# Kernel optimization log

Hardware: AMD Instinct MI355X
Metric: run time of the kernel (lower is better)

Reference implementation:

```python
import jax, jax.numpy as jnp
import numpy as np

N = 100000
E = 3200000
IN_DIM = 3
HID = 256
OUT_DIM = 3


def setup_inputs() -> dict:
    key = jax.random.key(0)
    ks = jax.random.split(key, 12)
    x = jax.random.normal(ks[0], (N, IN_DIM), dtype=jnp.float32)
    edge_index = jax.random.randint(ks[1], (2, E), 0, N, dtype=jnp.int64)
    def lin(k, fi, fo):
        k1, k2 = jax.random.split(k)
        bound = 1.0 / np.sqrt(fi)
        W = jax.random.uniform(k1, (fi, fo), jnp.float32, -bound, bound)
        b = jax.random.uniform(k2, (fo,), jnp.float32, -bound, bound)
        return W, b
    W0, b0 = lin(ks[2], IN_DIM, HID)
    W1, b1 = lin(ks[3], HID, HID)
    W2, b2 = lin(ks[4], HID, HID)
    W3, b3 = lin(ks[5], HID, OUT_DIM)
    Wr, br = lin(ks[6], IN_DIM, OUT_DIM)
    return {"x": x, "edge_index": edge_index,
            "W0": W0, "b0": b0, "W1": W1, "b1": b1,
            "W2": W2, "b2": b2, "W3": W3, "b3": b3,
            "Wr": Wr, "br": br}


def reference(x, edge_index, W0, b0, W1, b1, W2, b2, W3, b3, Wr, br):
    n = x.shape[0]
    # add self loops, mirroring build_adjacency_matrix
    loops = jnp.arange(n, dtype=edge_index.dtype)
    row = jnp.concatenate([edge_index[0], loops])
    col = jnp.concatenate([edge_index[1], loops])
    # degree of row endpoints, D^{-1/2}[row] * D^{-1/2}[col] edge weights
    deg = jax.ops.segment_sum(jnp.ones_like(row, dtype=x.dtype), row, num_segments=n)
    dinv = jnp.where(deg > 0, jax.lax.rsqrt(deg), 0.0)
    norm = dinv[row] * dinv[col]  # [E+N]

    def propagate(h):
        # A_hat @ h : gather source features, scale, scatter-add to rows
        return jax.ops.segment_sum(norm[:, None] * h[col], row, num_segments=n)

    h = jax.nn.relu(propagate(x) @ W0 + b0)
    h = jax.nn.relu(propagate(h) @ W1 + b1)
    h = jax.nn.relu(propagate(h) @ W2 + b2)
    h = propagate(h) @ W3 + b3  # last layer: no relu
    return h + (x @ Wr + br)
```

## Files before the change

### kernel.cpp

```cpp
#include <hip/hip_runtime.h>
#include <stdint.h>

typedef unsigned short u16;
typedef unsigned int u32;
typedef __attribute__((ext_vector_type(8))) short short8;
typedef __attribute__((ext_vector_type(4))) float f32x4;
typedef __attribute__((ext_vector_type(2))) unsigned int u32x2;

#define CAP 6144
#define TILE 4096

__device__ __forceinline__ float b2f_bits(u32 bits){ union{u32 u; float f;} v; v.u=bits; return v.f; }
__device__ __forceinline__ float bf_lo(u32 w){ return b2f_bits(w<<16); }
__device__ __forceinline__ float bf_hi(u32 w){ return b2f_bits(w & 0xffff0000u); }
__device__ __forceinline__ u16 f2bf(float f){
  union{float f; u32 u;} v; v.f=f;
  return (u16)((v.u + 0x7fffu + ((v.u>>16)&1u))>>16);
}


__global__ void detect_k(const long long* __restrict__ ei, int* __restrict__ flag,
                         int* __restrict__ gcur, int n, int E, int nbuck){
  __shared__ int sh[256];
  int t = threadIdx.x;
  for(int i=t; i<nbuck; i+=256) gcur[i]=0;
  int lim = E/2 < 2048 ? E/2 : 2048;
  int bad = 0;
  for(int e=t; e<lim; e+=256){
    unsigned long long v = (unsigned long long)ei[e];
    if(v >= (unsigned long long)n) bad = 1;
  }
  sh[t]=bad; __syncthreads();
  for(int off=128; off>0; off>>=1){ if(t<off) sh[t] |= sh[t+off]; __syncthreads(); }
  if(t==0) *flag = sh[0];
}

__device__ __forceinline__ int edge_at(const void* eiv, int is32, long long idx){
  return is32 ? ((const int*)eiv)[idx] : (int)((const long long*)eiv)[idx];
}
__device__ __forceinline__ int clampi(int v, int lo, int hi){
  return v < lo ? lo : (v > hi ? hi : v);
}

__global__ __launch_bounds__(256) void binA_k(const void* __restrict__ eiv, const int* __restrict__ flag,
                        int* __restrict__ gcur, u32* __restrict__ gbuf, int E, int n, int nbuck){
  __shared__ int hist[1024];
  __shared__ int base[1024];
  __shared__ int cur[1024];
  __shared__ int wsum[256];
  __shared__ u32 stage[TILE];
  int t = threadIdx.x;
  long long e0 = (long long)blockIdx.x * TILE;
  int cnt = (int)((long long)E - e0 < TILE ? (long long)E - e0 : TILE);
  int is32 = *flag;
  for(int i=t; i<nbuck; i+=256){ hist[i]=0; cur[i]=0; }
  __syncthreads();
  int eb[16]; u32 ep[16]; int ec=0;
  #pragma unroll
  for(int k=0;k<16;k++){
    int i = t + k*256;
    if(i<cnt){
      long long e = e0 + i;
      int r = clampi(edge_at(eiv,is32,e),0,n-1);
      int c = clampi(edge_at(eiv,is32,(long long)E+e),0,n-1);
      eb[ec] = r>>7;
      ep[ec] = ((u32)(r&127)<<17) | (u32)c;
      atomicAdd(&hist[eb[ec]],1);
      ec++;
    }
  }
  __syncthreads();
  int l[4]; int tot=0;
  #pragma unroll
  for(int j=0;j<4;j++){ int idx=t*4+j; l[j]=(idx<nbuck)?hist[idx]:0; tot+=l[j]; }
  wsum[t]=tot; __syncthreads();
  for(int off=1;off<256;off<<=1){
    int x = (t>=off)?wsum[t-off]:0;
    __syncthreads();
    wsum[t]+=x;
    __syncthreads();
  }
  int excl = wsum[t]-tot;
  #pragma unroll
  for(int j=0;j<4;j++){ int idx=t*4+j; if(idx<nbuck) base[idx]=excl; excl+=l[j]; }
  __syncthreads();
  for(int k=0;k<ec;k++){
    int b = eb[k];
    int slot = base[b] + atomicAdd(&cur[b],1);
    stage[slot] = ep[k];
  }
  __syncthreads();
  for(int b=t; b<nbuck; b+=256){
    int c = hist[b];
    if(c>0){
      int g = atomicAdd(&gcur[b], c);
      if(g > CAP) g = CAP;
      if(g + c > CAP) c = CAP - g;
      int src = base[b];
      u32* dst = gbuf + (size_t)b*CAP + g;
      for(int k=0;k<c;k++) dst[k] = stage[src+k];
    }
  }
}

__global__ __launch_bounds__(256) void scanG_k(const int* __restrict__ gcnt, int* __restrict__ gstart, int nbuck){
  __shared__ int sh[256];
  int t = threadIdx.x;
  int v[4]; int s=0;
  #pragma unroll
  for(int j=0;j<4;j++){
    int idx=t*4+j;
    int c = (idx<nbuck)?gcnt[idx]:0;
    if(c>CAP) c=CAP;
    v[j]=c; s+=c;
  }
  sh[t]=s; __syncthreads();
  for(int off=1;off<256;off<<=1){
    int x=(t>=off)?sh[t-off]:0;
    __syncthreads();
    sh[t]+=x;
    __syncthreads();
  }
  int excl = sh[t]-s;
  #pragma unroll
  for(int j=0;j<4;j++){ int idx=t*4+j; if(idx<nbuck) gstart[idx]=excl; excl+=v[j]; }
}

__global__ __launch_bounds__(256) void csrB_k(const int* __restrict__ gcnt, const int* __restrict__ gstart,
                        const u32* __restrict__ gbuf, int* __restrict__ deg, float* __restrict__ dinv,
                        int* __restrict__ rs, int* __restrict__ csr, int n, int nbuck){
  __shared__ int h[128], lst[128], lcur[128], sc[128];
  __shared__ int colstage[CAP];
  int b = blockIdx.x, t = threadIdx.x;
  if(t<128){ h[t]=0; lcur[t]=0; }
  __syncthreads();
  int c = gcnt[b]; if(c>CAP) c=CAP;
  const u32* p = gbuf + (size_t)b*CAP;
  for(int i=t;i<c;i+=256) atomicAdd(&h[p[i]>>17],1);
  __syncthreads();
  int dv=0;
  if(t<128){ dv=h[t]; sc[t]=dv; }
  __syncthreads();
  for(int off=1;off<128;off<<=1){
    int x=(t>=off&&t<128)?sc[t-off]:0;
    __syncthreads();
    if(t<128) sc[t]+=x;
    __syncthreads();
  }
  int g0 = gstart[b];
  if(t<128){
    lst[t]=sc[t]-dv;
    int row=b*128+t;
    if(row<n){
      deg[row]=dv;
      dinv[row]=rsqrtf((float)(dv+1));
      rs[row]=g0+lst[t];
    }
  }
  __syncthreads();
  for(int i=t;i<c;i+=256){
    u32 pr=p[i];
    int rl=pr>>17;
    int slot=lst[rl]+atomicAdd(&lcur[rl],1);
    if(slot<CAP) colstage[slot]=(int)(pr&0x1FFFFu);
  }
  __syncthreads();
  for(int i=t;i<c;i+=256) csr[g0+i]=colstage[i];
}

__global__ void pack2_k(const float* __restrict__ W1, const float* __restrict__ W2,
                        u16* __restrict__ o1, u16* __restrict__ o2){
  int bid = blockIdx.x;
  const float* W = (bid<256)? W1 : W2;
  u16* out = (bid<256)? o1 : o2;
  int idx = (bid&255)*256 + threadIdx.x;
  int j  = idx & 7;
  int l  = (idx>>3) & 63;
  int ct = (idx>>9) & 15;
  int kk = idx>>13;
  int k  = kk*32 + (l>>4)*8 + j;
  int nn = ct*16 + (l&15);
  out[idx] = f2bf(W[k*256 + nn]);
}

__global__ void prop3_k(const float* __restrict__ x, const int* __restrict__ csr,
                        const int* __restrict__ rs, const int* __restrict__ deg,
                        const float* __restrict__ dinv, float* __restrict__ p0, int n){
  int i = blockIdx.x*256 + threadIdx.x;
  if(i>=n) return;
  float a0=0.f, a1=0.f, a2=0.f;
  int s = rs[i], e = s + deg[i];
  for(int t=s; t<e; t++){
    int c = csr[t];
    float w = dinv[c];
    a0 += w*x[c*3+0]; a1 += w*x[c*3+1]; a2 += w*x[c*3+2];
  }
  float di = dinv[i];
  a0 += di*x[i*3+0]; a1 += di*x[i*3+1]; a2 += di*x[i*3+2];
  p0[i*3+0]=di*a0; p0[i*3+1]=di*a1; p0[i*3+2]=di*a2;
}

__global__ __launch_bounds__(256) void prop256_k(const u16* __restrict__ hin, u16* __restrict__ pout,
                          const int* __restrict__ csr, const int* __restrict__ rs,
                          const int* __restrict__ deg, const float* __restrict__ dinv, int n){
  int row = (blockIdx.x*256 + threadIdx.x) >> 6;
  if(row>=n) return;
  row = __builtin_amdgcn_readfirstlane(row);
  int lane = threadIdx.x & 63;
  int co = lane*4;
  const u16* hb = hin + co;
  uint2 sv = *(const uint2*)(hb + (size_t)row*256);
  float a0=bf_lo(sv.x), a1=bf_hi(sv.x), a2=bf_lo(sv.y), a3=bf_hi(sv.y);
  int s = __builtin_amdgcn_readfirstlane(rs[row]);
  int d = __builtin_amdgcn_readfirstlane(deg[row]);
  for(int base=0; base<d; base+=16){
    int cc[16]; u32 mk[16];
    #pragma unroll
    for(int j=0;j<16;j++){
      int ok = (base+j) < d;
      cc[j] = csr[ok ? (s+base+j) : s];
      mk[j] = ok ? 0xffffffffu : 0u;
    }
    uint2 v[16];
    #pragma unroll
    for(int j=0;j<16;j++) v[j] = *(const uint2*)(hb + (size_t)cc[j]*256);
    #pragma unroll
    for(int j=0;j<16;j++){
      u32 xw = v[j].x & mk[j], yw = v[j].y & mk[j];
      a0 += bf_lo(xw); a1 += bf_hi(xw); a2 += bf_lo(yw); a3 += bf_hi(yw);
    }
  }
  float sc = dinv[row];
  u32x2 o;
  o.x = (u32)f2bf(a0*sc) | ((u32)f2bf(a1*sc)<<16);
  o.y = (u32)f2bf(a2*sc) | ((u32)f2bf(a3*sc)<<16);
  __builtin_nontemporal_store(o, (u32x2*)(pout + (size_t)row*256 + co));
}

__global__ __launch_bounds__(256) void gemm0_k(const float* __restrict__ p0, const float* __restrict__ W0,
                        const float* __restrict__ b0, const float* __restrict__ dinv,
                        u16* __restrict__ h1, int n){
  int i = blockIdx.x;
  int j = threadIdx.x;
  float v = p0[i*3+0]*W0[j] + p0[i*3+1]*W0[256+j] + p0[i*3+2]*W0[512+j] + b0[j];
  v = fmaxf(v, 0.f) * dinv[i];
  h1[(size_t)i*256 + j] = f2bf(v);
}

__global__ __launch_bounds__(256) void gemm256_k(const u16* __restrict__ A, const u16* __restrict__ Bp,
                          const float* __restrict__ bias, const float* __restrict__ dinv,
                          u16* __restrict__ Out, int M){
  int wave = threadIdx.x>>6, lane = threadIdx.x&63;
  int rowbase = blockIdx.x*64 + wave*16;
  f32x4 acc[16];
  #pragma unroll
  for(int t=0;t<16;t++){ acc[t][0]=0.f; acc[t][1]=0.f; acc[t][2]=0.f; acc[t][3]=0.f; }
  const u16* Ap = A + (size_t)(rowbase + (lane&15))*256 + ((lane>>4)*8);
  const u16* Bl = Bp + (size_t)lane*8;
  #pragma unroll
  for(int kk=0; kk<8; kk++){
    short8 af = __builtin_nontemporal_load((const short8*)(Ap + kk*32));
    const u16* bb = Bl + (size_t)kk*8192;
    #pragma unroll
    for(int t=0;t<16;t++){
      short8 bf = *(const short8*)(bb + t*512);
      acc[t] = __builtin_amdgcn_mfma_f32_16x16x32_bf16(af, bf, acc[t], 0, 0, 0);
    }
  }
  int r0 = rowbase + (lane>>4)*4;
  float dv[4]; bool ok[4];
  #pragma unroll
  for(int r=0;r<4;r++){ ok[r] = (r0+r) < M; dv[r] = ok[r] ? dinv[r0+r] : 0.f; }
  #pragma unroll
  for(int t=0;t<16;t++){
    int col = t*16 + (lane&15);
    float bc = bias[col];
    #pragma unroll
    for(int r=0;r<4;r++){
      if(ok[r]){
        float v = fmaxf(acc[t][r] + bc, 0.f) * dv[r];
        Out[(size_t)(r0+r)*256 + col] = f2bf(v);
      }
    }
  }
}

__global__ __launch_bounds__(256) void gemm3_k(const u16* __restrict__ h3, const float* __restrict__ W3,
                        float* __restrict__ qh, int n){
  __shared__ float w3s[768];
  for(int i=threadIdx.x; i<768; i+=256) w3s[i] = W3[i];
  __syncthreads();
  int i = blockIdx.x*256 + threadIdx.x;
  if(i>=n) return;
  float a0=0.f, a1=0.f, a2=0.f;
  const uint4* hp = (const uint4*)(h3 + (size_t)i*256);
  for(int kk=0; kk<32; kk++){
    uint4 v = hp[kk];
    float f[8] = {bf_lo(v.x),bf_hi(v.x),bf_lo(v.y),bf_hi(v.y),
                  bf_lo(v.z),bf_hi(v.z),bf_lo(v.w),bf_hi(v.w)};
    int k0 = kk*8;
    #pragma unroll
    for(int j=0;j<8;j++){
      a0 += f[j]*w3s[(k0+j)*3+0];
      a1 += f[j]*w3s[(k0+j)*3+1];
      a2 += f[j]*w3s[(k0+j)*3+2];
    }
  }
  qh[i*3+0]=a0; qh[i*3+1]=a1; qh[i*3+2]=a2;
}

__global__ void final_k(const float* __restrict__ qh, const float* __restrict__ x,
                        const int* __restrict__ csr, const int* __restrict__ rs,
                        const int* __restrict__ deg, const float* __restrict__ dinv,
                        const float* __restrict__ b3, const float* __restrict__ Wr,
                        const float* __restrict__ br, float* __restrict__ out, int n){
  int i = blockIdx.x*256 + threadIdx.x;
  if(i>=n) return;
  float a0=0.f, a1=0.f, a2=0.f;
  int s = rs[i], e = s + deg[i];
  for(int t=s; t<e; t++){
    int c = csr[t];
    a0 += qh[c*3+0]; a1 += qh[c*3+1]; a2 += qh[c*3+2];
  }
  float di = dinv[i];
  a0 = di*(a0 + qh[i*3+0]);
  a1 = di*(a1 + qh[i*3+1]);
  a2 = di*(a2 + qh[i*3+2]);
  float x0=x[i*3+0], x1=x[i*3+1], x2=x[i*3+2];
  out[i*3+0] = a0 + b3[0] + x0*Wr[0] + x1*Wr[3] + x2*Wr[6] + br[0];
  out[i*3+1] = a1 + b3[1] + x0*Wr[1] + x1*Wr[4] + x2*Wr[7] + br[1];
  out[i*3+2] = a2 + b3[2] + x0*Wr[2] + x1*Wr[5] + x2*Wr[8] + br[2];
}

extern "C" void kernel_launch(void* const* d_in, const int* in_sizes, int n_in,
                              void* d_out, int out_size, void* d_ws, size_t ws_size,
                              hipStream_t stream) {
  const float* x  = (const float*)d_in[0];
  const void*  ei = d_in[1];
  const float* W0 = (const float*)d_in[2];
  const float* b0 = (const float*)d_in[3];
  const float* W1 = (const float*)d_in[4];
  const float* b1 = (const float*)d_in[5];
  const float* W2 = (const float*)d_in[6];
  const float* b2 = (const float*)d_in[7];
  const float* W3 = (const float*)d_in[8];
  const float* b3 = (const float*)d_in[9];
  const float* Wr = (const float*)d_in[10];
  const float* br = (const float*)d_in[11];
  float* out = (float*)d_out;

  int n = in_sizes[0]/3;
  int E = in_sizes[1]/2;
  int nbuck = (n+127)>>7;
  int Mpad = ((n+63)/64)*64;

  char* p = (char*)d_ws;
  auto alloc = [&](size_t bytes)->char*{ char* r=p; p += (bytes+255)&~(size_t)255; return r; };
  int*   gcur  = (int*)  alloc((size_t)nbuck*4);
  int*   gstart= (int*)  alloc((size_t)nbuck*4);
  int*   deg   = (int*)  alloc((size_t)n*4);
  float* dinv  = (float*)alloc((size_t)n*4);
  int*   rs    = (int*)  alloc((size_t)n*4);
  int*   flag  = (int*)  alloc(256);
  int*   csr   = (int*)  alloc((size_t)E*4);
  u16*   hA    = (u16*)  alloc((size_t)Mpad*512);
  u16*   hB    = (u16*)  alloc((size_t)Mpad*512);
  float* p0    = (float*)alloc((size_t)n*12);
  float* qh    = (float*)alloc((size_t)n*12);
  u16*   W1p   = (u16*)  alloc(65536*2);
  u16*   W2p   = (u16*)  alloc(65536*2);
  u32*   gbuf  = (u32*)hA;

  int gn  = (n+255)/256;
  int gA  = (E+TILE-1)/TILE;
  int gp  = (n*64+255)/256;

  detect_k<<<1, 256, 0, stream>>>((const long long*)ei, flag, gcur, n, E, nbuck);
  binA_k  <<<gA, 256, 0, stream>>>(ei, flag, gcur, gbuf, E, n, nbuck);
  scanG_k <<<1, 256, 0, stream>>>(gcur, gstart, nbuck);
  csrB_k  <<<nbuck, 256, 0, stream>>>(gcur, gstart, gbuf, deg, dinv, rs, csr, n, nbuck);

  pack2_k <<<512, 256, 0, stream>>>(W1, W2, W1p, W2p);

  prop3_k <<<gn, 256, 0, stream>>>(x, csr, rs, deg, dinv, p0, n);
  gemm0_k <<<n, 256, 0, stream>>>(p0, W0, b0, dinv, hA, n);

  prop256_k<<<gp, 256, 0, stream>>>(hA, hB, csr, rs, deg, dinv, n);
  gemm256_k<<<Mpad/64, 256, 0, stream>>>(hB, W1p, b1, dinv, hA, n);

  prop256_k<<<gp, 256, 0, stream>>>(hA, hB, csr, rs, deg, dinv, n);
  gemm256_k<<<Mpad/64, 256, 0, stream>>>(hB, W2p, b2, dinv, hA, n);

  gemm3_k <<<gn, 256, 0, stream>>>(hA, W3, qh, n);
  final_k <<<gn, 256, 0, stream>>>(qh, x, csr, rs, deg, dinv, b3, Wr, br, out, n);
}
```

Baseline: 879.0 us.

## Fuse layer-0 propagate with its GEMM, fuse W3 projection into last GEMM

Merges the 3-wide propagation and the first dense layer into one kernel with a block-per-row reduction. It also folds the 256x3 W3 projection into the epilogue of the second MFMA GEMM using shuffle reductions, so the third hidden activation is never written to or read back from memory. The final propagation now uses one wave per row with a lane-parallel neighbour loop instead of one thread per row, which targets the load imbalance of the serial per-thread loop. The cost is a block-wide shared-memory tree reduction per node in layer 0, with 256 threads on rows averaging about 32 edges, so most threads sit idle.

```diff
diff --git a/kernel.cpp b/kernel.cpp
--- a/kernel.cpp
+++ b/kernel.cpp
@@ -183,21 +183,36 @@
   out[idx] = f2bf(W[k*256 + nn]);
 }
 
-__global__ void prop3_k(const float* __restrict__ x, const int* __restrict__ csr,
+__global__ __launch_bounds__(256) void gemm0f_k(const float* __restrict__ x, const int* __restrict__ csr,
                         const int* __restrict__ rs, const int* __restrict__ deg,
-                        const float* __restrict__ dinv, float* __restrict__ p0, int n){
-  int i = blockIdx.x*256 + threadIdx.x;
-  if(i>=n) return;
+                        const float* __restrict__ dinv, const float* __restrict__ W0,
+                        const float* __restrict__ b0, u16* __restrict__ h1, int n){
+  __shared__ float s0[256], s1[256], s2[256];
+  __shared__ float pr[3];
+  int i = blockIdx.x;
+  int t = threadIdx.x;
+  int s = rs[i], d = deg[i];
   float a0=0.f, a1=0.f, a2=0.f;
-  int s = rs[i], e = s + deg[i];
-  for(int t=s; t<e; t++){
-    int c = csr[t];
+  for(int e=t; e<d; e+=256){
+    int c = csr[s+e];
     float w = dinv[c];
     a0 += w*x[c*3+0]; a1 += w*x[c*3+1]; a2 += w*x[c*3+2];
   }
-  float di = dinv[i];
-  a0 += di*x[i*3+0]; a1 += di*x[i*3+1]; a2 += di*x[i*3+2];
-  p0[i*3+0]=di*a0; p0[i*3+1]=di*a1; p0[i*3+2]=di*a2;
+  s0[t]=a0; s1[t]=a1; s2[t]=a2; __syncthreads();
+  for(int off=128; off>0; off>>=1){
+    if(t<off){ s0[t]+=s0[t+off]; s1[t]+=s1[t+off]; s2[t]+=s2[t+off]; }
+    __syncthreads();
+  }
+  if(t==0){
+    float di = dinv[i];
+    pr[0] = di*(s0[0] + di*x[i*3+0]);
+    pr[1] = di*(s1[0] + di*x[i*3+1]);
+    pr[2] = di*(s2[0] + di*x[i*3+2]);
+  }
+  __syncthreads();
+  float v = pr[0]*W0[t] + pr[1]*W0[256+t] + pr[2]*W0[512+t] + b0[t];
+  v = fmaxf(v, 0.f) * dinv[i];
+  h1[(size_t)i*256 + t] = f2bf(v);
 }
 
 __global__ __launch_bounds__(256) void prop256_k(const u16* __restrict__ hin, u16* __restrict__ pout,
@@ -237,16 +252,6 @@
   __builtin_nontemporal_store(o, (u32x2*)(pout + (size_t)row*256 + co));
 }
 
-__global__ __launch_bounds__(256) void gemm0_k(const float* __restrict__ p0, const float* __restrict__ W0,
-                        const float* __restrict__ b0, const float* __restrict__ dinv,
-                        u16* __restrict__ h1, int n){
-  int i = blockIdx.x;
-  int j = threadIdx.x;
-  float v = p0[i*3+0]*W0[j] + p0[i*3+1]*W0[256+j] + p0[i*3+2]*W0[512+j] + b0[j];
-  v = fmaxf(v, 0.f) * dinv[i];
-  h1[(size_t)i*256 + j] = f2bf(v);
-}
-
 __global__ __launch_bounds__(256) void gemm256_k(const u16* __restrict__ A, const u16* __restrict__ Bp,
                           const float* __restrict__ bias, const float* __restrict__ dinv,
                           u16* __restrict__ Out, int M){
@@ -285,51 +290,98 @@
   }
 }
 
-__global__ __launch_bounds__(256) void gemm3_k(const u16* __restrict__ h3, const float* __restrict__ W3,
-                        float* __restrict__ qh, int n){
+__global__ __launch_bounds__(256) void gemm256w3_k(const u16* __restrict__ A, const u16* __restrict__ Bp,
+                          const float* __restrict__ bias, const float* __restrict__ dinv,
+                          const float* __restrict__ W3, float* __restrict__ qh, int M){
   __shared__ float w3s[768];
   for(int i=threadIdx.x; i<768; i+=256) w3s[i] = W3[i];
   __syncthreads();
-  int i = blockIdx.x*256 + threadIdx.x;
-  if(i>=n) return;
-  float a0=0.f, a1=0.f, a2=0.f;
-  const uint4* hp = (const uint4*)(h3 + (size_t)i*256);
-  for(int kk=0; kk<32; kk++){
-    uint4 v = hp[kk];
-    float f[8] = {bf_lo(v.x),bf_hi(v.x),bf_lo(v.y),bf_hi(v.y),
-                  bf_lo(v.z),bf_hi(v.z),bf_lo(v.w),bf_hi(v.w)};
-    int k0 = kk*8;
-    #pragma unroll
-    for(int j=0;j<8;j++){
-      a0 += f[j]*w3s[(k0+j)*3+0];
-      a1 += f[j]*w3s[(k0+j)*3+1];
-      a2 += f[j]*w3s[(k0+j)*3+2];
-    }
-  }
-  qh[i*3+0]=a0; qh[i*3+1]=a1; qh[i*3+2]=a2;
-}
-
-__global__ void final_k(const float* __restrict__ qh, const float* __restrict__ x,
+  int wave = threadIdx.x>>6, lane = threadIdx.x&63;
+  int rowbase = blockIdx.x*64 + wave*16;
+  f32x4 acc[16];
+  #pragma unroll
+  for(int t=0;t<16;t++){ acc[t][0]=0.f; acc[t][1]=0.f; acc[t][2]=0.f; acc[t][3]=0.f; }
+  const u16* Ap = A + (size_t)(rowbase + (lane&15))*256 + ((lane>>4)*8);
+  const u16* Bl = Bp + (size_t)lane*8;
+  #pragma unroll
+  for(int kk=0; kk<8; kk++){
+    short8 af = __builtin_nontemporal_load((const short8*)(Ap + kk*32));
+    const u16* bb = Bl + (size_t)kk*8192;
+    #pragma unroll
+    for(int t=0;t<16;t++){
+      short8 bf = *(const short8*)(bb + t*512);
+      acc[t] = __builtin_amdgcn_mfma_f32_16x16x32_bf16(af, bf, acc[t], 0, 0, 0);
+    }
+  }
+  int r0 = rowbase + (lane>>4)*4;
+  int cl = lane & 15;
+  float dv[4];
+  #pragma unroll
+  for(int r=0;r<4;r++) dv[r] = (r0+r) < M ? dinv[r0+r] : 0.f;
+  float q0[4]={0,0,0,0}, q1[4]={0,0,0,0}, q2[4]={0,0,0,0};
+  #pragma unroll
+  for(int t=0;t<16;t++){
+    int col = t*16 + cl;
+    float bc = bias[col];
+    float w30=w3s[col*3+0], w31=w3s[col*3+1], w32=w3s[col*3+2];
+    #pragma unroll
+    for(int r=0;r<4;r++){
+      float v = fmaxf(acc[t][r] + bc, 0.f) * dv[r];
+      q0[r] += v*w30; q1[r] += v*w31; q2[r] += v*w32;
+    }
+  }
+  #pragma unroll
+  for(int off=1; off<16; off<<=1){
+    #pragma unroll
+    for(int r=0;r<4;r++){
+      q0[r] += __shfl_xor(q0[r], off);
+      q1[r] += __shfl_xor(q1[r], off);
+      q2[r] += __shfl_xor(q2[r], off);
+    }
+  }
+  if(cl==0){
+    #pragma unroll
+    for(int r=0;r<4;r++){
+      int row = r0 + r;
+      if(row < M){
+        qh[row*3+0]=q0[r]; qh[row*3+1]=q1[r]; qh[row*3+2]=q2[r];
+      }
+    }
+  }
+}
+
+__global__ __launch_bounds__(256) void final2_k(const float* __restrict__ qh, const float* __restrict__ x,
                         const int* __restrict__ csr, const int* __restrict__ rs,
                         const int* __restrict__ deg, const float* __restrict__ dinv,
                         const float* __restrict__ b3, const float* __restrict__ Wr,
                         const float* __restrict__ br, float* __restrict__ out, int n){
-  int i = blockIdx.x*256 + threadIdx.x;
-  if(i>=n) return;
+  int row = (blockIdx.x*256 + threadIdx.x) >> 6;
+  if(row>=n) return;
+  row = __builtin_amdgcn_readfirstlane(row);
+  int lane = threadIdx.x & 63;
+  int s = __builtin_amdgcn_readfirstlane(rs[row]);
+  int d = __builtin_amdgcn_readfirstlane(deg[row]);
   float a0=0.f, a1=0.f, a2=0.f;
-  int s = rs[i], e = s + deg[i];
-  for(int t=s; t<e; t++){
-    int c = csr[t];
+  for(int e=lane; e<d; e+=64){
+    int c = csr[s+e];
     a0 += qh[c*3+0]; a1 += qh[c*3+1]; a2 += qh[c*3+2];
   }
-  float di = dinv[i];
-  a0 = di*(a0 + qh[i*3+0]);
-  a1 = di*(a1 + qh[i*3+1]);
-  a2 = di*(a2 + qh[i*3+2]);
-  float x0=x[i*3+0], x1=x[i*3+1], x2=x[i*3+2];
-  out[i*3+0] = a0 + b3[0] + x0*Wr[0] + x1*Wr[3] + x2*Wr[6] + br[0];
-  out[i*3+1] = a1 + b3[1] + x0*Wr[1] + x1*Wr[4] + x2*Wr[7] + br[1];
-  out[i*3+2] = a2 + b3[2] + x0*Wr[2] + x1*Wr[5] + x2*Wr[8] + br[2];
+  #pragma unroll
+  for(int off=32; off>0; off>>=1){
+    a0 += __shfl_xor(a0, off);
+    a1 += __shfl_xor(a1, off);
+    a2 += __shfl_xor(a2, off);
+  }
+  if(lane==0){
+    float di = dinv[row];
+    a0 = di*(a0 + qh[row*3+0]);
+    a1 = di*(a1 + qh[row*3+1]);
+    a2 = di*(a2 + qh[row*3+2]);
+    float x0=x[row*3+0], x1=x[row*3+1], x2=x[row*3+2];
+    out[row*3+0] = a0 + b3[0] + x0*Wr[0] + x1*Wr[3] + x2*Wr[6] + br[0];
+    out[row*3+1] = a1 + b3[1] + x0*Wr[1] + x1*Wr[4] + x2*Wr[7] + br[1];
+    out[row*3+2] = a2 + b3[2] + x0*Wr[2] + x1*Wr[5] + x2*Wr[8] + br[2];
+  }
 }
 
 extern "C" void kernel_launch(void* const* d_in, const int* in_sizes, int n_in,
@@ -365,13 +417,11 @@
   int*   csr   = (int*)  alloc((size_t)E*4);
   u16*   hA    = (u16*)  alloc((size_t)Mpad*512);
   u16*   hB    = (u16*)  alloc((size_t)Mpad*512);
-  float* p0    = (float*)alloc((size_t)n*12);
   float* qh    = (float*)alloc((size_t)n*12);
   u16*   W1p   = (u16*)  alloc(65536*2);
   u16*   W2p   = (u16*)  alloc(65536*2);
   u32*   gbuf  = (u32*)hA;
 
-  int gn  = (n+255)/256;
   int gA  = (E+TILE-1)/TILE;
   int gp  = (n*64+255)/256;
 
@@ -382,15 +432,13 @@
 
   pack2_k <<<512, 256, 0, stream>>>(W1, W2, W1p, W2p);
 
-  prop3_k <<<gn, 256, 0, stream>>>(x, csr, rs, deg, dinv, p0, n);
-  gemm0_k <<<n, 256, 0, stream>>>(p0, W0, b0, dinv, hA, n);
+  gemm0f_k<<<n, 256, 0, stream>>>(x, csr, rs, deg, dinv, W0, b0, hA, n);
 
   prop256_k<<<gp, 256, 0, stream>>>(hA, hB, csr, rs, deg, dinv, n);
   gemm256_k<<<Mpad/64, 256, 0, stream>>>(hB, W1p, b1, dinv, hA, n);
 
   prop256_k<<<gp, 256, 0, stream>>>(hA, hB, csr, rs, deg, dinv, n);
-  gemm256_k<<<Mpad/64, 256, 0, stream>>>(hB, W2p, b2, dinv, hA, n);
-
-  gemm3_k <<<gn, 256, 0, stream>>>(hA, W3, qh, n);
-  final_k <<<gn, 256, 0, stream>>>(qh, x, csr, rs, deg, dinv, b3, Wr, br, out, n);
-}
+  gemm256w3_k<<<Mpad/64, 256, 0, stream>>>(hB, W2p, b2, dinv, W3, qh, n);
+
+  final2_k<<<gp, 256, 0, stream>>>(qh, x, csr, rs, deg, dinv, b3, Wr, br, out, n);
+}
```

Result: no change. 875.9 us (-0.4%).
